# Performance work log

Hardware: AMD Instinct MI355X
Metric: run time of the kernel (lower is better)

## Reference

```python
import jax, jax.numpy as jnp
import numpy as np

DIM, SEQ, HEADS, HDIM, BATCH, VOCAB, NVOCAB = 512, 1024, 8, 64, 8, 1024, 3
EPS = 1e-5


def layer_norm(x, g, b):
    mu = x.mean(-1, keepdims=True)
    var = x.var(-1, keepdims=True)
    return (x - mu) * jax.lax.rsqrt(var + EPS) * g + b


def multiscale_retention(x, Wq, Wk, Wv, Wg, Wo):
    B, S, D = x.shape
    def split(h):  # [B,S,D] -> [B,H,S,hd]
        return h.reshape(B, S, HEADS, HDIM).transpose(0, 2, 1, 3)
    q, k, v = split(x @ Wq), split(x @ Wk), split(x @ Wv)
    # RetNet per-head decays and causal decay matrix D[h,n,m] = gamma_h^(n-m), n>=m
    gammas = 1.0 - 2.0 ** (-5.0 - jnp.arange(HEADS, dtype=jnp.float32))
    n = jnp.arange(S)
    diff = n[:, None] - n[None, :]
    decay = jnp.where(diff >= 0, gammas[:, None, None] ** jnp.maximum(diff, 0).astype(jnp.float32), 0.0)
    scores = jnp.einsum('bhsd,bhtd->bhst', q, k) * (1.0 / np.sqrt(HDIM))
    y = jnp.einsum('bhst,bhtd->bhsd', scores * decay, v)
    # group norm per head (no affine)
    mu = y.mean(-1, keepdims=True)
    var = y.var(-1, keepdims=True)
    y = (y - mu) * jax.lax.rsqrt(var + EPS)
    y = y.transpose(0, 2, 1, 3).reshape(B, S, D)
    gate = jax.nn.swish(x @ Wg)
    return (gate * y) @ Wo


def feed_forward(x, W1, b1, W2, b2):
    return jax.nn.relu(x @ W1 + b1) @ W2 + b2


def setup_inputs() -> dict:
    key = jax.random.key(0)
    ks = jax.random.split(key, 12)
    s = 0.02
    return {
        'ids': jax.random.randint(ks[0], (NVOCAB, BATCH, SEQ), 0, VOCAB),
        'emb_tables': jax.random.normal(ks[1], (NVOCAB, VOCAB, DIM), jnp.float32) * s,
        'pos_emb': jax.random.normal(ks[2], (NVOCAB, SEQ, DIM), jnp.float32) * s,
        'ln_gamma': jnp.ones((DIM,), jnp.float32),
        'ln_beta': jnp.zeros((DIM,), jnp.float32),
        'Wq': jax.random.normal(ks[3], (DIM, DIM), jnp.float32) * s,
        'Wk': jax.random.normal(ks[4], (DIM, DIM), jnp.float32) * s,
        'Wv': jax.random.normal(ks[5], (DIM, DIM), jnp.float32) * s,
        'Wg': jax.random.normal(ks[6], (DIM, DIM), jnp.float32) * s,
        'Wo': jax.random.normal(ks[7], (DIM, DIM), jnp.float32) * s,
        'W1': jax.random.normal(ks[8], (DIM, DIM), jnp.float32) * s,
        'b1': jnp.zeros((DIM,), jnp.float32),
        'W2': jax.random.normal(ks[9], (DIM, DIM), jnp.float32) * s,
        'b2': jnp.zeros((DIM,), jnp.float32),
        'fc_W': jax.random.normal(ks[10], (SEQ * DIM, 1), jnp.float32) * s,
        'fc_b': jnp.zeros((1,), jnp.float32),
    }


def reference(ids, emb_tables, pos_emb, ln_gamma, ln_beta, Wq, Wk, Wv, Wg, Wo,
              W1, b1, W2, b2, fc_W, fc_b):
    x = None
    for i in range(NVOCAB):  # loop over vocab embeddings, x overwritten each pass (as in source)
        emb = emb_tables[i][ids[i]] + pos_emb[i][None, :, :]  # [B,S,D]
        x = layer_norm(emb, ln_gamma, ln_beta)
        x = multiscale_retention(x, Wq, Wk, Wv, Wg, Wo) + x
        x = feed_forward(layer_norm(x, ln_gamma, ln_beta), W1, b1, W2, b2) + x
        x = layer_norm(x, ln_gamma, ln_beta)
    flat = x.reshape(x.shape[0], -1)  # Flatten
    return jax.nn.sigmoid(flat @ fc_W + fc_b)  # dropout inactive at inference
```

## Files before the change

### kernel.cpp

```cpp
#include <hip/hip_runtime.h>
#include <math.h>

typedef unsigned short u16;
typedef __attribute__((ext_vector_type(8))) _Float16 half8;
typedef __attribute__((ext_vector_type(4))) float f32x4;
typedef __attribute__((ext_vector_type(4))) unsigned short us4;


static __device__ __forceinline__ u16 f2h(float f) {
    _Float16 h = (_Float16)f;
    return __builtin_bit_cast(u16, h);
}
static __device__ __forceinline__ float h2f(u16 u) {
    return (float)__builtin_bit_cast(_Float16, u);
}
static __device__ __forceinline__ void gl_lds16(const void* g, void* l) {
    __builtin_amdgcn_global_load_lds(
        (const __attribute__((address_space(1))) void*)g,
        (__attribute__((address_space(3))) void*)l, 16, 0, 0);
}

__global__ __launch_bounds__(256) void prep_kernel(
    const float* __restrict__ Wq, const float* __restrict__ Wk, const float* __restrict__ Wv,
    const float* __restrict__ Wg, const float* __restrict__ Wo, const float* __restrict__ W1,
    const float* __restrict__ W2, u16* __restrict__ WT,
    const int* __restrict__ ids, const float* __restrict__ emb, const float* __restrict__ pos,
    const float* __restrict__ gam, const float* __restrict__ bet, u16* __restrict__ x0h)
{
    __shared__ float tile[64][65];
    int bx = blockIdx.x, t = threadIdx.x;
    if (bx < 448) {
        const float* Ws[7] = {Wq, Wk, Wv, Wg, Wo, W1, W2};
        int w = bx >> 6, rem = bx & 63;
        int k0 = (rem >> 3) * 64, n0 = (rem & 7) * 64;
        const float* W = Ws[w];
        for (int c = t; c < 4096; c += 256) {
            int row = c >> 6, col = c & 63;
            tile[row][col] = W[(size_t)(k0 + row) * 512 + n0 + col];
        }
        __syncthreads();
        for (int c = t; c < 4096; c += 256) {
            int row = c >> 6, col = c & 63;
            WT[(size_t)w * 262144 + (size_t)(n0 + row) * 512 + k0 + col] = f2h(tile[col][row]);
        }
    } else {
        int wid = t >> 6, lane = t & 63;
        int rbase = (bx - 448) * 8 + wid * 2;
        int col = lane * 8;
        int id0 = ids[2 * 8192 + rbase];
        int id1 = ids[2 * 8192 + rbase + 1];
        const float* pp0 = pos + (size_t)(2 * 1024 + (rbase & 1023)) * 512 + col;
        const float* pp1 = pos + (size_t)(2 * 1024 + ((rbase + 1) & 1023)) * 512 + col;
        float4 pa0 = *(const float4*)pp0, pa1 = *(const float4*)(pp0 + 4);
        float4 pb0 = *(const float4*)pp1, pb1 = *(const float4*)(pp1 + 4);
        float4 g0 = *(const float4*)&gam[col], g1 = *(const float4*)&gam[col + 4];
        float4 c0 = *(const float4*)&bet[col], c1 = *(const float4*)&bet[col + 4];
        const float* ep0 = emb + (size_t)(2 * 1024 + id0) * 512 + col;
        const float* ep1 = emb + (size_t)(2 * 1024 + id1) * 512 + col;
        float4 ea0 = *(const float4*)ep0, ea1 = *(const float4*)(ep0 + 4);
        float4 eb0 = *(const float4*)ep1, eb1 = *(const float4*)(ep1 + 4);

        float va[8] = {ea0.x + pa0.x, ea0.y + pa0.y, ea0.z + pa0.z, ea0.w + pa0.w,
                       ea1.x + pa1.x, ea1.y + pa1.y, ea1.z + pa1.z, ea1.w + pa1.w};
        float vb[8] = {eb0.x + pb0.x, eb0.y + pb0.y, eb0.z + pb0.z, eb0.w + pb0.w,
                       eb1.x + pb1.x, eb1.y + pb1.y, eb1.z + pb1.z, eb1.w + pb1.w};
        float s1a = 0.f, s2a = 0.f, s1b = 0.f, s2b = 0.f;
#pragma unroll
        for (int j = 0; j < 8; ++j) {
            s1a += va[j]; s2a += va[j] * va[j];
            s1b += vb[j]; s2b += vb[j] * vb[j];
        }
#pragma unroll
        for (int o = 32; o >= 1; o >>= 1) {
            s1a += __shfl_xor(s1a, o, 64);
            s2a += __shfl_xor(s2a, o, 64);
            s1b += __shfl_xor(s1b, o, 64);
            s2b += __shfl_xor(s2b, o, 64);
        }
        float mua = s1a * (1.f / 512.f);
        float vara = fmaxf(s2a * (1.f / 512.f) - mua * mua, 0.f);
        float rsa = 1.f / sqrtf(vara + 1e-5f);
        float mub = s1b * (1.f / 512.f);
        float varb = fmaxf(s2b * (1.f / 512.f) - mub * mub, 0.f);
        float rsb = 1.f / sqrtf(varb + 1e-5f);
        float gv[8] = {g0.x, g0.y, g0.z, g0.w, g1.x, g1.y, g1.z, g1.w};
        float bv[8] = {c0.x, c0.y, c0.z, c0.w, c1.x, c1.y, c1.z, c1.w};
        half8 ha, hb;
#pragma unroll
        for (int j = 0; j < 8; ++j) {
            ha[j] = (_Float16)((va[j] - mua) * rsa * gv[j] + bv[j]);
            hb[j] = (_Float16)((vb[j] - mub) * rsb * gv[j] + bv[j]);
        }
        *(half8*)&x0h[(size_t)rbase * 512 + col] = ha;
        *(half8*)&x0h[(size_t)(rbase + 1) * 512 + col] = hb;
    }
}

__global__ __launch_bounds__(256) void ln_kernel(
    const u16* __restrict__ xin,
    const float* __restrict__ gam, const float* __restrict__ bet,
    u16* __restrict__ outh,
    const float* __restrict__ fcW, float* __restrict__ fcpart)
{
    int wid = threadIdx.x >> 6, lane = threadIdx.x & 63;
    int row = blockIdx.x * 4 + wid;
    int col = lane * 8;
    float v[8];
    half8 x = *(const half8*)&xin[(size_t)row * 512 + col];
#pragma unroll
    for (int j = 0; j < 8; ++j) v[j] = (float)x[j];
    float s1 = 0.f, s2 = 0.f;
#pragma unroll
    for (int j = 0; j < 8; ++j) { s1 += v[j]; s2 += v[j] * v[j]; }
#pragma unroll
    for (int o = 32; o >= 1; o >>= 1) {
        s1 += __shfl_xor(s1, o, 64);
        s2 += __shfl_xor(s2, o, 64);
    }
    float mu = s1 * (1.f / 512.f);
    float var = fmaxf(s2 * (1.f / 512.f) - mu * mu, 0.f);
    float rs = 1.f / sqrtf(var + 1e-5f);
    float4 g0 = *(const float4*)&gam[col], g1 = *(const float4*)&gam[col + 4];
    float4 b0 = *(const float4*)&bet[col], b1 = *(const float4*)&bet[col + 4];
    float gv[8] = {g0.x, g0.y, g0.z, g0.w, g1.x, g1.y, g1.z, g1.w};
    float bv[8] = {b0.x, b0.y, b0.z, b0.w, b1.x, b1.y, b1.z, b1.w};
    float y[8];
#pragma unroll
    for (int j = 0; j < 8; ++j) y[j] = (v[j] - mu) * rs * gv[j] + bv[j];
    if (outh) {
        half8 hv;
#pragma unroll
        for (int j = 0; j < 8; ++j) hv[j] = (_Float16)y[j];
        *(half8*)&outh[(size_t)row * 512 + col] = hv;
    }
    if (fcW) {
        int srow = row & 1023;
        const float* wp = &fcW[(size_t)srow * 512 + col];
        float4 w0 = *(const float4*)wp, w1 = *(const float4*)(wp + 4);
        float d = y[0] * w0.x + y[1] * w0.y + y[2] * w0.z + y[3] * w0.w +
                  y[4] * w1.x + y[5] * w1.y + y[6] * w1.z + y[7] * w1.w;
#pragma unroll
        for (int o = 32; o >= 1; o >>= 1) d += __shfl_xor(d, o, 64);
        if (lane == 0) fcpart[row] = d;
    }
}

static __device__ __forceinline__ void stage_tile(
    const u16* pa0, const u16* pa1, const u16* pb0, const u16* pb1,
    u16* ldsw, int slot, int kt)
{
    int off = kt * 32;
    u16* d = ldsw + slot * 16384;
    gl_lds16(pa0 + off, d);
    gl_lds16(pa1 + off, d + 4096);
    gl_lds16(pb0 + off, d + 8192);
    gl_lds16(pb1 + off, d + 12288);
}

static __device__ __forceinline__ void compute_tile(
    const u16* lds, int slot, int wm, int wn, int quad, int l15, f32x4 (&acc)[8][4])
{
    const u16* A = lds + slot * 16384;
    const u16* B = A + 8192;
    __builtin_amdgcn_s_setprio(1);
#pragma unroll
    for (int mq = 0; mq < 2; ++mq)
#pragma unroll
        for (int nq = 0; nq < 2; ++nq) {
            half8 a[4], b[2];
#pragma unroll
            for (int i = 0; i < 4; ++i)
                a[i] = *(const half8*)&A[(wm * 128 + mq * 64 + i * 16 + l15) * 32 + quad * 8];
#pragma unroll
            for (int j = 0; j < 2; ++j)
                b[j] = *(const half8*)&B[(wn * 64 + nq * 32 + j * 16 + l15) * 32 + quad * 8];
#pragma unroll
            for (int i = 0; i < 4; ++i)
#pragma unroll
                for (int j = 0; j < 2; ++j)
                    acc[mq * 4 + i][nq * 2 + j] = __builtin_amdgcn_mfma_f32_16x16x32_f16(
                        a[i], b[j], acc[mq * 4 + i][nq * 2 + j], 0, 0, 0);
        }
    __builtin_amdgcn_s_setprio(0);
}

#define QITER(KT, VM)                                                              \
    do {                                                                           \
        if ((KT) + 3 < 16) stage_tile(pa0, pa1, pb0, pb1, ldsw, ((KT) + 3) & 3, (KT) + 3); \
        asm volatile("s_waitcnt vmcnt(" #VM ")" ::: "memory");                     \
        __builtin_amdgcn_s_barrier();                                              \
        asm volatile("" ::: "memory");                                             \
        compute_tile(lds, (KT) & 3, wm, wn, quad, l15, acc);                       \
        asm volatile("" ::: "memory");                                             \
        __builtin_amdgcn_s_barrier();                                              \
    } while (0)

__global__ __launch_bounds__(512, 2) void gemm_f16(
    const u16* __restrict__ A2, const u16* __restrict__ Bg,
    u16* __restrict__ outh, int ostride)
{
    __shared__ u16 lds[65536];
    int t = threadIdx.x;
    int wid = t >> 6, lane = t & 63, quad = lane >> 4, l15 = lane & 15;
    int wm = wid >> 2, wn = wid & 3;
    int orig = blockIdx.x;
    int wgid = (orig & 7) * 32 + (orig >> 3);
    int m0 = (wgid >> 3) * 256, n0 = (wgid & 7) * 256;

    int srow = t >> 2, sc = (t & 3) * 8;
    const u16* pa0 = A2 + (size_t)(m0 + srow) * 512 + sc;
    const u16* pa1 = pa0 + (size_t)128 * 512;
    const u16* pb0 = Bg + (size_t)(n0 + srow) * 512 + sc;
    const u16* pb1 = pb0 + (size_t)128 * 512;
    u16* ldsw = lds + wid * 512;

    f32x4 acc[8][4];
#pragma unroll
    for (int i = 0; i < 8; ++i)
#pragma unroll
        for (int j = 0; j < 4; ++j) acc[i][j] = (f32x4){0.f, 0.f, 0.f, 0.f};

    stage_tile(pa0, pa1, pb0, pb1, ldsw, 0, 0);
    stage_tile(pa0, pa1, pb0, pb1, ldsw, 1, 1);
    stage_tile(pa0, pa1, pb0, pb1, ldsw, 2, 2);

    QITER(0, 12);  QITER(1, 12);  QITER(2, 12);  QITER(3, 12);
    QITER(4, 12);  QITER(5, 12);  QITER(6, 12);  QITER(7, 12);
    QITER(8, 12);  QITER(9, 12);  QITER(10, 12); QITER(11, 12);
    QITER(12, 12);
    QITER(13, 8);  QITER(14, 4);  QITER(15, 0);

    u16* C = lds;
#pragma unroll
    for (int i = 0; i < 8; ++i)
#pragma unroll
        for (int j = 0; j < 4; ++j)
#pragma unroll
            for (int r = 0; r < 4; ++r)
                C[(wm * 128 + i * 16 + quad * 4 + r) * 256 + wn * 64 + j * 16 + l15] =
                    f2h(acc[i][j][r]);
    __builtin_amdgcn_s_barrier();
    asm volatile("" ::: "memory");
#pragma unroll
    for (int it = 0; it < 16; ++it) {
        int idx = it * 512 + t;
        int row = idx >> 5, ch = idx & 31;
        *(half8*)&outh[(size_t)(m0 + row) * ostride + n0 + ch * 8] =
            *(const half8*)&C[row * 256 + ch * 8];
    }
}

static __device__ __forceinline__ void stage_n64(
    const u16* pa, const u16* pb, u16* ldsw, int slot, int kt)
{
    int off = kt * 32;
    u16* d = ldsw + slot * 8192;
    gl_lds16(pa + off, d);
    gl_lds16(pb + off, d + 4096);
}

static __device__ __forceinline__ void compute_n64(
    const u16* lds, int slot, int wm, int wn, int quad, int l15, f32x4 (&acc)[4][2])
{
    const u16* A = lds + slot * 8192;
    const u16* B = A + 4096;
    __builtin_amdgcn_s_setprio(1);
    half8 a[4], b[2];
#pragma unroll
    for (int i = 0; i < 4; ++i)
        a[i] = *(const half8*)&A[(wm * 64 + i * 16 + l15) * 32 + quad * 8];
#pragma unroll
    for (int j = 0; j < 2; ++j)
        b[j] = *(const half8*)&B[(wn * 32 + j * 16 + l15) * 32 + quad * 8];
#pragma unroll
    for (int i = 0; i < 4; ++i)
#pragma unroll
        for (int j = 0; j < 2; ++j)
            acc[i][j] = __builtin_amdgcn_mfma_f32_16x16x32_f16(a[i], b[j], acc[i][j], 0, 0, 0);
    __builtin_amdgcn_s_setprio(0);
}

#define NITER(KT, VM)                                                          \
    do {                                                                       \
        if ((KT) + 3 < 16) stage_n64(pa, pb, ldsw, ((KT) + 3) & 3, (KT) + 3);  \
        asm volatile("s_waitcnt vmcnt(" #VM ")" ::: "memory");                 \
        __builtin_amdgcn_s_barrier();                                          \
        asm volatile("" ::: "memory");                                         \
        compute_n64(lds, (KT) & 3, wm, wn, quad, l15, acc);                    \
        asm volatile("" ::: "memory");                                         \
        __builtin_amdgcn_s_barrier();                                          \
    } while (0)

__global__ __launch_bounds__(512, 2) void gemm_f16_n64(
    const u16* __restrict__ A2, const u16* __restrict__ Bg,
    u16* __restrict__ outh,
    const u16* __restrict__ res, const float* __restrict__ bias, int mode)
{
    __shared__ u16 lds[32768];
    int t = threadIdx.x;
    int wid = t >> 6, lane = t & 63, quad = lane >> 4, l15 = lane & 15;
    int wm = wid >> 2, wn = wid & 3;
    int orig = blockIdx.x;
    int wgid = (orig & 7) * 32 + (orig >> 3);
    int m0 = (wgid >> 2) * 128, n0 = (wgid & 3) * 128;

    int srow = t >> 2, sc = (t & 3) * 8;
    const u16* pa = A2 + (size_t)(m0 + srow) * 512 + sc;
    const u16* pb = Bg + (size_t)(n0 + srow) * 512 + sc;
    u16* ldsw = lds + wid * 512;

    f32x4 acc[4][2];
#pragma unroll
    for (int i = 0; i < 4; ++i)
#pragma unroll
        for (int j = 0; j < 2; ++j) acc[i][j] = (f32x4){0.f, 0.f, 0.f, 0.f};

    stage_n64(pa, pb, ldsw, 0, 0);
    stage_n64(pa, pb, ldsw, 1, 1);
    stage_n64(pa, pb, ldsw, 2, 2);

    NITER(0, 6);  NITER(1, 6);  NITER(2, 6);  NITER(3, 6);
    NITER(4, 6);  NITER(5, 6);  NITER(6, 6);  NITER(7, 6);
    NITER(8, 6);  NITER(9, 6);  NITER(10, 6); NITER(11, 6);
    NITER(12, 6);
    NITER(13, 4); NITER(14, 2); NITER(15, 0);

#pragma unroll
    for (int i = 0; i < 4; ++i)
#pragma unroll
        for (int j = 0; j < 2; ++j) {
            int nl = wn * 32 + j * 16 + l15;
            int n = n0 + nl;
#pragma unroll
            for (int r = 0; r < 4; ++r) {
                int rl = wm * 64 + i * 16 + quad * 4 + r;
                int m = m0 + rl;
                float v = acc[i][j][r];
                if (mode == 1) v += h2f(res[(size_t)m * 512 + n]);
                else if (mode == 2) v = fmaxf(v + bias[n], 0.f);
                else if (mode == 3) v += bias[n] + h2f(res[(size_t)m * 512 + n]);
                lds[rl * 128 + nl] = f2h(v);
            }
        }
    __builtin_amdgcn_s_barrier();
    asm volatile("" ::: "memory");
#pragma unroll
    for (int it = 0; it < 4; ++it) {
        int idx = it * 512 + t;
        int row = idx >> 4, ch = idx & 15;
        *(half8*)&outh[(size_t)(m0 + row) * 512 + n0 + ch * 8] =
            *(const half8*)&lds[row * 128 + ch * 8];
    }
}

__global__ __launch_bounds__(256) void chunk_t(
    const u16* __restrict__ QKVGh, u16* __restrict__ Tst)
{
    __shared__ u16 kth[64 * 144];
    __shared__ u16 vth[64 * 144];
    int t = threadIdx.x;
    int wid = t >> 6, lane = t & 63, quad = lane >> 4, l15 = lane & 15;
    int bh = blockIdx.x >> 3, c = blockIdx.x & 7;
    int b = bh >> 3, h = bh & 7;
    float gamma = 1.f - exp2f(-(float)(5 + h));
    float l2g = log2f(gamma);

    for (int cc = t; cc < 2048; cc += 256) {
        int d = cc & 63, mseg = cc >> 6;
        size_t gbase = (size_t)(b * 1024 + c * 128 + mseg * 4) * 2048 + h * 64 + d;
        us4 k4, v4;
#pragma unroll
        for (int i = 0; i < 4; ++i) {
            float kv = h2f(QKVGh[gbase + 512 + (size_t)i * 2048]);
            k4[i] = f2h(kv * exp2f((float)(127 - (mseg * 4 + i)) * l2g));
            v4[i] = QKVGh[gbase + 1024 + (size_t)i * 2048];
        }
        int base = d * 144 + (((mseg >> 1) + d) & 15) * 8 + (mseg & 1) * 4;
        *(us4*)&kth[base] = k4;
        *(us4*)&vth[base] = v4;
    }
    __syncthreads();
    f32x4 T[4];
#pragma unroll
    for (int dt = 0; dt < 4; ++dt) T[dt] = (f32x4){0.f, 0.f, 0.f, 0.f};
    int ra = wid * 16 + l15;
#pragma unroll
    for (int ks = 0; ks < 4; ++ks) {
        half8 av = *(const half8*)&vth[ra * 144 + ((ks * 4 + quad + ra) & 15) * 8];
#pragma unroll
        for (int dt = 0; dt < 4; ++dt) {
            int rb = dt * 16 + l15;
            half8 bk = *(const half8*)&kth[rb * 144 + ((ks * 4 + quad + rb) & 15) * 8];
            T[dt] = __builtin_amdgcn_mfma_f32_16x16x32_f16(av, bk, T[dt], 0, 0, 0);
        }
    }
#pragma unroll
    for (int dt = 0; dt < 4; ++dt)
#pragma unroll
        for (int r = 0; r < 4; ++r) {
            int i = wid * 16 + quad * 4 + r;
            int j = dt * 16 + l15;
            Tst[(((size_t)bh * 8 + c) * 64 + i) * 64 + j] = f2h(T[dt][r]);
        }
}

__global__ __launch_bounds__(256) void retention_f16(
    const u16* __restrict__ QKVGh, const u16* __restrict__ Tst, u16* __restrict__ Zh)
{
    __shared__ u16 kh[128 * 64];
    __shared__ u16 vth[64 * 144];
    __shared__ u16 ph[4][16 * 132];

    int t = threadIdx.x;
    int wid = t >> 6, lane = t & 63, quad = lane >> 4, l15 = lane & 15;
    int bh = blockIdx.x >> 3, qt = blockIdx.x & 7;
    int b = bh >> 3, h = bh & 7;
    int n0 = qt * 128;

    float gamma = 1.f - exp2f(-(float)(5 + h));
    float l2g = log2f(gamma);

    {
        int srow = wid * 8 + (lane >> 3);
        int scol = (lane & 7) * 8;
#pragma unroll
        for (int i = 0; i < 4; ++i) {
            int r = i * 32 + srow;
            gl_lds16(&QKVGh[(size_t)(b * 1024 + n0 + r) * 2048 + 512 + h * 64 + scol],
                     &kh[(i * 32 + wid * 8) * 64]);
        }
    }
    for (int c = t; c < 2048; c += 256) {
        int d = c & 63, mseg = c >> 6;
        size_t gbase = (size_t)(b * 1024 + n0 + mseg * 4) * 2048 + 1024 + h * 64 + d;
        us4 v4 = {QKVGh[gbase], QKVGh[gbase + 2048],
                  QKVGh[gbase + 4096], QKVGh[gbase + 6144]};
        int base = d * 144 + (((mseg >> 1) + d) & 15) * 8 + (mseg & 1) * 4;
        *(us4*)&vth[base] = v4;
    }

    half8 aH[2][2], aHs[2][2];
#pragma unroll
    for (int g = 0; g < 2; ++g) {
        int rowloc = wid * 32 + g * 16 + l15;
        int qrow = b * 1024 + n0 + rowloc;
        const u16* qp = QKVGh + (size_t)qrow * 2048 + h * 64;
        float qs = exp2f((float)(rowloc + 1) * l2g - 3.f);
#pragma unroll
        for (int ks = 0; ks < 2; ++ks) {
            aH[g][ks] = *(const half8*)&qp[ks * 32 + quad * 8];
#pragma unroll
            for (int j = 0; j < 8; ++j)
                aHs[g][ks][j] = (_Float16)((float)aH[g][ks][j] * qs);
        }
    }

    half8 sf[2][4];
    if (qt > 0) {
        float sa[2][4][8];
#pragma unroll
        for (int ks = 0; ks < 2; ++ks)
#pragma unroll
            for (int dt = 0; dt < 4; ++dt)
#pragma unroll
                for (int j = 0; j < 8; ++j) sa[ks][dt][j] = 0.f;
        for (int c = 0; c < qt; ++c) {
            float sc = exp2f((float)(128 * (qt - 1 - c)) * l2g);
            const u16* tp = &Tst[((size_t)bh * 8 + c) * 4096];
#pragma unroll
            for (int ks = 0; ks < 2; ++ks)
#pragma unroll
                for (int dt = 0; dt < 4; ++dt) {
                    half8 tv = *(const half8*)&tp[(dt * 16 + l15) * 64 + ks * 32 + quad * 8];
#pragma unroll
                    for (int j = 0; j < 8; ++j) sa[ks][dt][j] += sc * (float)tv[j];
                }
        }
#pragma unroll
        for (int ks = 0; ks < 2; ++ks)
#pragma unroll
            for (int dt = 0; dt < 4; ++dt)
#pragma unroll
                for (int j = 0; j < 8; ++j) sf[ks][dt][j] = (_Float16)sa[ks][dt][j];
    }
    __syncthreads();

    f32x4 yacc[2][4];
#pragma unroll
    for (int g = 0; g < 2; ++g)
#pragma unroll
        for (int dt = 0; dt < 4; ++dt) yacc[g][dt] = (f32x4){0.f, 0.f, 0.f, 0.f};

    if (qt > 0) {
#pragma unroll
        for (int ks = 0; ks < 2; ++ks)
#pragma unroll
            for (int g = 0; g < 2; ++g)
#pragma unroll
                for (int dt = 0; dt < 4; ++dt)
                    yacc[g][dt] = __builtin_amdgcn_mfma_f32_16x16x32_f16(aHs[g][ks], sf[ks][dt], yacc[g][dt], 0, 0, 0);
    }

#pragma unroll
    for (int g = 0; g < 2; ++g) {
        f32x4 sacc[8];
#pragma unroll
        for (int tn = 0; tn < 8; ++tn) sacc[tn] = (f32x4){0.f, 0.f, 0.f, 0.f};
#pragma unroll
        for (int tn = 0; tn < 8; ++tn)
#pragma unroll
            for (int ks = 0; ks < 2; ++ks) {
                half8 bH = *(const half8*)&kh[(tn * 16 + l15) * 64 + ks * 32 + quad * 8];
                sacc[tn] = __builtin_amdgcn_mfma_f32_16x16x32_f16(aH[g][ks], bH, sacc[tn], 0, 0, 0);
            }
#pragma unroll
        for (int tn = 0; tn < 8; ++tn) {
            int mloc = tn * 16 + l15;
#pragma unroll
            for (int r = 0; r < 4; ++r) {
                int nloc = wid * 32 + g * 16 + quad * 4 + r;
                int diff = nloc - mloc;
                float p = (diff >= 0) ? sacc[tn][r] * exp2f((float)diff * l2g - 3.0f) : 0.f;
                ph[wid][(quad * 4 + r) * 132 + tn * 16 + l15] = f2h(p);
            }
        }
        half8 pH[4];
#pragma unroll
        for (int ks = 0; ks < 4; ++ks)
            pH[ks] = *(const half8*)&ph[wid][l15 * 132 + ks * 32 + quad * 8];
#pragma unroll
        for (int dt = 0; dt < 4; ++dt) {
            int d = dt * 16 + l15;
#pragma unroll
            for (int ks = 0; ks < 4; ++ks) {
                half8 vv = *(const half8*)&vth[d * 144 + ((ks * 4 + quad + d) & 15) * 8];
                yacc[g][dt] = __builtin_amdgcn_mfma_f32_16x16x32_f16(pH[ks], vv, yacc[g][dt], 0, 0, 0);
            }
        }
    }

#pragma unroll
    for (int g = 0; g < 2; ++g) {
#pragma unroll
        for (int r = 0; r < 4; ++r) {
            float s1 = yacc[g][0][r] + yacc[g][1][r] + yacc[g][2][r] + yacc[g][3][r];
            float s2 = yacc[g][0][r] * yacc[g][0][r] + yacc[g][1][r] * yacc[g][1][r] +
                       yacc[g][2][r] * yacc[g][2][r] + yacc[g][3][r] * yacc[g][3][r];
#pragma unroll
            for (int o = 1; o <= 8; o <<= 1) {
                s1 += __shfl_xor(s1, o, 64);
                s2 += __shfl_xor(s2, o, 64);
            }
            float mu = s1 * (1.f / 64.f);
            float var = fmaxf(s2 * (1.f / 64.f) - mu * mu, 0.f);
            float rs = 1.f / sqrtf(var + 1e-5f);
            int nglob = n0 + wid * 32 + g * 16 + quad * 4 + r;
            size_t grow = (size_t)(b * 1024 + nglob);
#pragma unroll
            for (int dt = 0; dt < 4; ++dt) {
                int d = dt * 16 + l15;
                float yv = (yacc[g][dt][r] - mu) * rs;
                float gt = h2f(QKVGh[grow * 2048 + 1536 + h * 64 + d]);
                float sw = gt / (1.f + expf(-gt));
                Zh[grow * 512 + h * 64 + d] = f2h(yv * sw);
            }
        }
    }
}

__global__ __launch_bounds__(256) void fc_final(const float* __restrict__ fcpart,
                                                const float* __restrict__ fcb,
                                                float* __restrict__ out)
{
    __shared__ float red[4];
    int b = blockIdx.x, t = threadIdx.x;
    float4 v = *(const float4*)&fcpart[(size_t)b * 1024 + t * 4];
    float s = v.x + v.y + v.z + v.w;
    int wid = t >> 6, lane = t & 63;
#pragma unroll
    for (int o = 32; o >= 1; o >>= 1) s += __shfl_xor(s, o, 64);
    if (lane == 0) red[wid] = s;
    __syncthreads();
    if (t == 0) {
        float l = red[0] + red[1] + red[2] + red[3] + fcb[0];
        out[b] = 1.f / (1.f + expf(-l));
    }
}

extern "C" void kernel_launch(void* const* d_in, const int* in_sizes, int n_in,
                              void* d_out, int out_size, void* d_ws, size_t ws_size,
                              hipStream_t stream)
{
    const int* ids = (const int*)d_in[0];
    const float* emb = (const float*)d_in[1];
    const float* pos = (const float*)d_in[2];
    const float* ln_g = (const float*)d_in[3];
    const float* ln_b = (const float*)d_in[4];
    const float* Wq = (const float*)d_in[5];
    const float* Wk = (const float*)d_in[6];
    const float* Wv = (const float*)d_in[7];
    const float* Wg = (const float*)d_in[8];
    const float* Wo = (const float*)d_in[9];
    const float* W1 = (const float*)d_in[10];
    const float* b1 = (const float*)d_in[11];
    const float* W2 = (const float*)d_in[12];
    const float* b2 = (const float*)d_in[13];
    const float* fcW = (const float*)d_in[14];
    const float* fcb = (const float*)d_in[15];
    float* out = (float*)d_out;

    char* ws = (char*)d_ws;
    u16* WT     = (u16*)(ws);
    u16* x0h    = (u16*)(ws + 3670016);
    u16* Zh     = (u16*)(ws + 12058624);
    u16* QKVGh  = (u16*)(ws + 20447232);
    float* fcpart = (float*)(ws + 54001664);
    u16* Tst    = (u16*)(ws + 54034432);
    u16* X1h = QKVGh;
    u16* Th  = (u16*)((char*)QKVGh + 8388608);
    u16* Hh  = (u16*)((char*)QKVGh + 16777216);
    u16* X2h = Zh;

    prep_kernel<<<1472, 256, 0, stream>>>(Wq, Wk, Wv, Wg, Wo, W1, W2, WT,
                                          ids, emb, pos, ln_g, ln_b, x0h);
    gemm_f16<<<256, 512, 0, stream>>>(x0h, WT, QKVGh, 2048);
    chunk_t<<<512, 256, 0, stream>>>(QKVGh, Tst);
    retention_f16<<<512, 256, 0, stream>>>(QKVGh, Tst, Zh);
    gemm_f16_n64<<<256, 512, 0, stream>>>(Zh, WT + 4 * 262144, X1h, x0h, nullptr, 1);
    ln_kernel<<<2048, 256, 0, stream>>>(X1h, ln_g, ln_b, Th, nullptr, nullptr);
    gemm_f16_n64<<<256, 512, 0, stream>>>(Th, WT + 5 * 262144, Hh, nullptr, b1, 2);
    gemm_f16_n64<<<256, 512, 0, stream>>>(Hh, WT + 6 * 262144, X2h, X1h, b2, 3);
    ln_kernel<<<2048, 256, 0, stream>>>(X2h, ln_g, ln_b, nullptr, fcW, fcpart);
    fc_final<<<8, 256, 0, stream>>>(fcpart, fcb, out);
}
```

Measured before the change: 208.8 us.

## Fuse post-retention GEMMs, layernorms and FC into one cooperative persistent kernel

```diff
diff --git a/kernel.cpp b/kernel.cpp
--- a/kernel.cpp
+++ b/kernel.cpp
@@ -1,5 +1,8 @@
 #include <hip/hip_runtime.h>
+#include <hip/hip_cooperative_groups.h>
 #include <math.h>
+
+namespace cg = cooperative_groups;
 
 typedef unsigned short u16;
 typedef __attribute__((ext_vector_type(8))) _Float16 half8;
@@ -96,55 +99,6 @@
     }
 }
 
-__global__ __launch_bounds__(256) void ln_kernel(
-    const u16* __restrict__ xin,
-    const float* __restrict__ gam, const float* __restrict__ bet,
-    u16* __restrict__ outh,
-    const float* __restrict__ fcW, float* __restrict__ fcpart)
-{
-    int wid = threadIdx.x >> 6, lane = threadIdx.x & 63;
-    int row = blockIdx.x * 4 + wid;
-    int col = lane * 8;
-    float v[8];
-    half8 x = *(const half8*)&xin[(size_t)row * 512 + col];
-#pragma unroll
-    for (int j = 0; j < 8; ++j) v[j] = (float)x[j];
-    float s1 = 0.f, s2 = 0.f;
-#pragma unroll
-    for (int j = 0; j < 8; ++j) { s1 += v[j]; s2 += v[j] * v[j]; }
-#pragma unroll
-    for (int o = 32; o >= 1; o >>= 1) {
-        s1 += __shfl_xor(s1, o, 64);
-        s2 += __shfl_xor(s2, o, 64);
-    }
-    float mu = s1 * (1.f / 512.f);
-    float var = fmaxf(s2 * (1.f / 512.f) - mu * mu, 0.f);
-    float rs = 1.f / sqrtf(var + 1e-5f);
-    float4 g0 = *(const float4*)&gam[col], g1 = *(const float4*)&gam[col + 4];
-    float4 b0 = *(const float4*)&bet[col], b1 = *(const float4*)&bet[col + 4];
-    float gv[8] = {g0.x, g0.y, g0.z, g0.w, g1.x, g1.y, g1.z, g1.w};
-    float bv[8] = {b0.x, b0.y, b0.z, b0.w, b1.x, b1.y, b1.z, b1.w};
-    float y[8];
-#pragma unroll
-    for (int j = 0; j < 8; ++j) y[j] = (v[j] - mu) * rs * gv[j] + bv[j];
-    if (outh) {
-        half8 hv;
-#pragma unroll
-        for (int j = 0; j < 8; ++j) hv[j] = (_Float16)y[j];
-        *(half8*)&outh[(size_t)row * 512 + col] = hv;
-    }
-    if (fcW) {
-        int srow = row & 1023;
-        const float* wp = &fcW[(size_t)srow * 512 + col];
-        float4 w0 = *(const float4*)wp, w1 = *(const float4*)(wp + 4);
-        float d = y[0] * w0.x + y[1] * w0.y + y[2] * w0.z + y[3] * w0.w +
-                  y[4] * w1.x + y[5] * w1.y + y[6] * w1.z + y[7] * w1.w;
-#pragma unroll
-        for (int o = 32; o >= 1; o >>= 1) d += __shfl_xor(d, o, 64);
-        if (lane == 0) fcpart[row] = d;
-    }
-}
-
 static __device__ __forceinline__ void stage_tile(
     const u16* pa0, const u16* pa1, const u16* pb0, const u16* pb1,
     u16* ldsw, int slot, int kt)
@@ -291,12 +245,12 @@
         __builtin_amdgcn_s_barrier();                                          \
     } while (0)
 
-__global__ __launch_bounds__(512, 2) void gemm_f16_n64(
+template <int MODE>
+static __device__ __forceinline__ void gemm_stage(
     const u16* __restrict__ A2, const u16* __restrict__ Bg,
-    u16* __restrict__ outh,
-    const u16* __restrict__ res, const float* __restrict__ bias, int mode)
-{
-    __shared__ u16 lds[32768];
+    u16* __restrict__ outh, const u16* __restrict__ res,
+    const float* __restrict__ bias, u16* lds)
+{
     int t = threadIdx.x;
     int wid = t >> 6, lane = t & 63, quad = lane >> 4, l15 = lane & 15;
     int wm = wid >> 2, wn = wid & 3;
@@ -336,9 +290,9 @@
                 int rl = wm * 64 + i * 16 + quad * 4 + r;
                 int m = m0 + rl;
                 float v = acc[i][j][r];
-                if (mode == 1) v += h2f(res[(size_t)m * 512 + n]);
-                else if (mode == 2) v = fmaxf(v + bias[n], 0.f);
-                else if (mode == 3) v += bias[n] + h2f(res[(size_t)m * 512 + n]);
+                if (MODE == 1) v += h2f(res[(size_t)m * 512 + n]);
+                else if (MODE == 2) v = fmaxf(v + bias[n], 0.f);
+                else if (MODE == 3) v += bias[n] + h2f(res[(size_t)m * 512 + n]);
                 lds[rl * 128 + nl] = f2h(v);
             }
         }
@@ -350,6 +304,97 @@
         int row = idx >> 4, ch = idx & 15;
         *(half8*)&outh[(size_t)(m0 + row) * 512 + n0 + ch * 8] =
             *(const half8*)&lds[row * 128 + ch * 8];
+    }
+}
+
+static __device__ __forceinline__ void ln_stage(
+    const u16* __restrict__ xin, const float* __restrict__ gam,
+    const float* __restrict__ bet, u16* __restrict__ outh,
+    const float* __restrict__ fcW, float* __restrict__ fcpart)
+{
+    int wid = threadIdx.x >> 6, lane = threadIdx.x & 63;
+    int col = lane * 8;
+    float4 g0 = *(const float4*)&gam[col], g1 = *(const float4*)&gam[col + 4];
+    float4 c0 = *(const float4*)&bet[col], c1 = *(const float4*)&bet[col + 4];
+    float gv[8] = {g0.x, g0.y, g0.z, g0.w, g1.x, g1.y, g1.z, g1.w};
+    float bv[8] = {c0.x, c0.y, c0.z, c0.w, c1.x, c1.y, c1.z, c1.w};
+#pragma unroll
+    for (int rr = 0; rr < 4; ++rr) {
+        int row = blockIdx.x * 32 + wid * 4 + rr;
+        float v[8];
+        half8 x = *(const half8*)&xin[(size_t)row * 512 + col];
+#pragma unroll
+        for (int j = 0; j < 8; ++j) v[j] = (float)x[j];
+        float s1 = 0.f, s2 = 0.f;
+#pragma unroll
+        for (int j = 0; j < 8; ++j) { s1 += v[j]; s2 += v[j] * v[j]; }
+#pragma unroll
+        for (int o = 32; o >= 1; o >>= 1) {
+            s1 += __shfl_xor(s1, o, 64);
+            s2 += __shfl_xor(s2, o, 64);
+        }
+        float mu = s1 * (1.f / 512.f);
+        float var = fmaxf(s2 * (1.f / 512.f) - mu * mu, 0.f);
+        float rs = 1.f / sqrtf(var + 1e-5f);
+        float y[8];
+#pragma unroll
+        for (int j = 0; j < 8; ++j) y[j] = (v[j] - mu) * rs * gv[j] + bv[j];
+        if (outh) {
+            half8 hv;
+#pragma unroll
+            for (int j = 0; j < 8; ++j) hv[j] = (_Float16)y[j];
+            *(half8*)&outh[(size_t)row * 512 + col] = hv;
+        }
+        if (fcW) {
+            int srow = row & 1023;
+            const float* wp = &fcW[(size_t)srow * 512 + col];
+            float4 w0 = *(const float4*)wp, w1 = *(const float4*)(wp + 4);
+            float d = y[0] * w0.x + y[1] * w0.y + y[2] * w0.z + y[3] * w0.w +
+                      y[4] * w1.x + y[5] * w1.y + y[6] * w1.z + y[7] * w1.w;
+#pragma unroll
+            for (int o = 32; o >= 1; o >>= 1) d += __shfl_xor(d, o, 64);
+            if (lane == 0) fcpart[row] = d;
+        }
+    }
+}
+
+__global__ __launch_bounds__(512, 2) void tail_fused(
+    const u16* __restrict__ Zh, const u16* __restrict__ WT,
+    const u16* __restrict__ x0h, u16* __restrict__ X1h,
+    u16* __restrict__ Th, u16* __restrict__ Hh, u16* __restrict__ X2h,
+    const float* __restrict__ b1v, const float* __restrict__ b2v,
+    const float* __restrict__ gam, const float* __restrict__ bet,
+    const float* __restrict__ fcW, float* __restrict__ fcpart,
+    const float* __restrict__ fcb, float* __restrict__ out)
+{
+    cg::grid_group grid = cg::this_grid();
+    __shared__ u16 lds[32768];
+
+    gemm_stage<1>(Zh, WT + 4 * 262144, X1h, x0h, nullptr, lds);
+    grid.sync();
+    ln_stage(X1h, gam, bet, Th, nullptr, nullptr);
+    grid.sync();
+    gemm_stage<2>(Th, WT + 5 * 262144, Hh, nullptr, b1v, lds);
+    grid.sync();
+    gemm_stage<3>(Hh, WT + 6 * 262144, X2h, X1h, b2v, lds);
+    grid.sync();
+    ln_stage(X2h, gam, bet, nullptr, fcW, fcpart);
+    grid.sync();
+    if (blockIdx.x < 8) {
+        int b = blockIdx.x, t = threadIdx.x;
+        float* red = (float*)lds;
+        float2 v = *(const float2*)&fcpart[(size_t)b * 1024 + t * 2];
+        float s = v.x + v.y;
+        int wid = t >> 6, lane = t & 63;
+#pragma unroll
+        for (int o = 32; o >= 1; o >>= 1) s += __shfl_xor(s, o, 64);
+        if (lane == 0) red[wid] = s;
+        __syncthreads();
+        if (t == 0) {
+            float l = red[0] + red[1] + red[2] + red[3] +
+                      red[4] + red[5] + red[6] + red[7] + fcb[0];
+            out[b] = 1.f / (1.f + expf(-l));
+        }
     }
 }
 
@@ -565,25 +610,6 @@
                 Zh[grow * 512 + h * 64 + d] = f2h(yv * sw);
             }
         }
-    }
-}
-
-__global__ __launch_bounds__(256) void fc_final(const float* __restrict__ fcpart,
-                                                const float* __restrict__ fcb,
-                                                float* __restrict__ out)
-{
-    __shared__ float red[4];
-    int b = blockIdx.x, t = threadIdx.x;
-    float4 v = *(const float4*)&fcpart[(size_t)b * 1024 + t * 4];
-    float s = v.x + v.y + v.z + v.w;
-    int wid = t >> 6, lane = t & 63;
-#pragma unroll
-    for (int o = 32; o >= 1; o >>= 1) s += __shfl_xor(s, o, 64);
-    if (lane == 0) red[wid] = s;
-    __syncthreads();
-    if (t == 0) {
-        float l = red[0] + red[1] + red[2] + red[3] + fcb[0];
-        out[b] = 1.f / (1.f + expf(-l));
     }
 }
 
@@ -626,10 +652,15 @@
     gemm_f16<<<256, 512, 0, stream>>>(x0h, WT, QKVGh, 2048);
     chunk_t<<<512, 256, 0, stream>>>(QKVGh, Tst);
     retention_f16<<<512, 256, 0, stream>>>(QKVGh, Tst, Zh);
-    gemm_f16_n64<<<256, 512, 0, stream>>>(Zh, WT + 4 * 262144, X1h, x0h, nullptr, 1);
-    ln_kernel<<<2048, 256, 0, stream>>>(X1h, ln_g, ln_b, Th, nullptr, nullptr);
-    gemm_f16_n64<<<256, 512, 0, stream>>>(Th, WT + 5 * 262144, Hh, nullptr, b1, 2);
-    gemm_f16_n64<<<256, 512, 0, stream>>>(Hh, WT + 6 * 262144, X2h, X1h, b2, 3);
-    ln_kernel<<<2048, 256, 0, stream>>>(X2h, ln_g, ln_b, nullptr, fcW, fcpart);
-    fc_final<<<8, 256, 0, stream>>>(fcpart, fcb, out);
-}
+
+    const u16* Zh_c = Zh;
+    const u16* WT_c = WT;
+    const u16* x0h_c = x0h;
+    void* args[] = {
+        (void*)&Zh_c, (void*)&WT_c, (void*)&x0h_c,
+        (void*)&X1h, (void*)&Th, (void*)&Hh, (void*)&X2h,
+        (void*)&b1, (void*)&b2, (void*)&ln_g, (void*)&ln_b,
+        (void*)&fcW, (void*)&fcpart, (void*)&fcb, (void*)&out};
+    hipLaunchCooperativeKernel((const void*)tail_fused, dim3(256), dim3(512),
+                               args, 0, stream);
+}
```

Measured after the change: 378.5 us. 1.81x slower.

## Precompute chunk state prefix scan in separate kernel for retention

Applied to the files above, without the earlier changes.

```diff
diff --git a/kernel.cpp b/kernel.cpp
--- a/kernel.cpp
+++ b/kernel.cpp
@@ -404,8 +404,28 @@
         }
 }
 
+__global__ __launch_bounds__(256) void tscan(
+    const u16* __restrict__ Tst, u16* __restrict__ Sst)
+{
+    int bh = blockIdx.x >> 3, p = blockIdx.x & 7;
+    int h = bh & 7;
+    float gamma = 1.f - exp2f(-(float)(5 + h));
+    float g128 = exp2f(128.f * log2f(gamma));
+    int e = p * 512 + threadIdx.x * 2;
+    const u16* tp = Tst + (size_t)bh * 32768 + e;
+    u16* sp = Sst + (size_t)bh * 32768 + e;
+    float s0 = 0.f, s1 = 0.f;
+#pragma unroll
+    for (int c = 0; c < 8; ++c) {
+        sp[c * 4096] = f2h(s0);
+        sp[c * 4096 + 1] = f2h(s1);
+        s0 = g128 * s0 + h2f(tp[c * 4096]);
+        s1 = g128 * s1 + h2f(tp[c * 4096 + 1]);
+    }
+}
+
 __global__ __launch_bounds__(256) void retention_f16(
-    const u16* __restrict__ QKVGh, const u16* __restrict__ Tst, u16* __restrict__ Zh)
+    const u16* __restrict__ QKVGh, const u16* __restrict__ Sst, u16* __restrict__ Zh)
 {
     __shared__ u16 kh[128 * 64];
     __shared__ u16 vth[64 * 144];
@@ -456,50 +476,29 @@
     }
 
     half8 sf[2][4];
-    if (qt > 0) {
-        float sa[2][4][8];
+    {
+        const u16* sp = &Sst[((size_t)bh * 8 + qt) * 4096];
 #pragma unroll
         for (int ks = 0; ks < 2; ++ks)
 #pragma unroll
             for (int dt = 0; dt < 4; ++dt)
-#pragma unroll
-                for (int j = 0; j < 8; ++j) sa[ks][dt][j] = 0.f;
-        for (int c = 0; c < qt; ++c) {
-            float sc = exp2f((float)(128 * (qt - 1 - c)) * l2g);
-            const u16* tp = &Tst[((size_t)bh * 8 + c) * 4096];
-#pragma unroll
-            for (int ks = 0; ks < 2; ++ks)
-#pragma unroll
-                for (int dt = 0; dt < 4; ++dt) {
-                    half8 tv = *(const half8*)&tp[(dt * 16 + l15) * 64 + ks * 32 + quad * 8];
-#pragma unroll
-                    for (int j = 0; j < 8; ++j) sa[ks][dt][j] += sc * (float)tv[j];
-                }
-        }
-#pragma unroll
-        for (int ks = 0; ks < 2; ++ks)
+                sf[ks][dt] = *(const half8*)&sp[(dt * 16 + l15) * 64 + ks * 32 + quad * 8];
+    }
+    __syncthreads();
+
+    f32x4 yacc[2][4];
+#pragma unroll
+    for (int g = 0; g < 2; ++g)
+#pragma unroll
+        for (int dt = 0; dt < 4; ++dt) yacc[g][dt] = (f32x4){0.f, 0.f, 0.f, 0.f};
+
+#pragma unroll
+    for (int ks = 0; ks < 2; ++ks)
+#pragma unroll
+        for (int g = 0; g < 2; ++g)
 #pragma unroll
             for (int dt = 0; dt < 4; ++dt)
-#pragma unroll
-                for (int j = 0; j < 8; ++j) sf[ks][dt][j] = (_Float16)sa[ks][dt][j];
-    }
-    __syncthreads();
-
-    f32x4 yacc[2][4];
-#pragma unroll
-    for (int g = 0; g < 2; ++g)
-#pragma unroll
-        for (int dt = 0; dt < 4; ++dt) yacc[g][dt] = (f32x4){0.f, 0.f, 0.f, 0.f};
-
-    if (qt > 0) {
-#pragma unroll
-        for (int ks = 0; ks < 2; ++ks)
-#pragma unroll
-            for (int g = 0; g < 2; ++g)
-#pragma unroll
-                for (int dt = 0; dt < 4; ++dt)
-                    yacc[g][dt] = __builtin_amdgcn_mfma_f32_16x16x32_f16(aHs[g][ks], sf[ks][dt], yacc[g][dt], 0, 0, 0);
-    }
+                yacc[g][dt] = __builtin_amdgcn_mfma_f32_16x16x32_f16(aHs[g][ks], sf[ks][dt], yacc[g][dt], 0, 0, 0);
 
 #pragma unroll
     for (int g = 0; g < 2; ++g) {
@@ -616,6 +615,7 @@
     u16* QKVGh  = (u16*)(ws + 20447232);
     float* fcpart = (float*)(ws + 54001664);
     u16* Tst    = (u16*)(ws + 54034432);
+    u16* Sst    = (u16*)(ws + 58228736);
     u16* X1h = QKVGh;
     u16* Th  = (u16*)((char*)QKVGh + 8388608);
     u16* Hh  = (u16*)((char*)QKVGh + 16777216);
@@ -625,7 +625,8 @@
                                           ids, emb, pos, ln_g, ln_b, x0h);
     gemm_f16<<<256, 512, 0, stream>>>(x0h, WT, QKVGh, 2048);
     chunk_t<<<512, 256, 0, stream>>>(QKVGh, Tst);
-    retention_f16<<<512, 256, 0, stream>>>(QKVGh, Tst, Zh);
+    tscan<<<512, 256, 0, stream>>>(Tst, Sst);
+    retention_f16<<<512, 256, 0, stream>>>(QKVGh, Sst, Zh);
     gemm_f16_n64<<<256, 512, 0, stream>>>(Zh, WT + 4 * 262144, X1h, x0h, nullptr, 1);
     ln_kernel<<<2048, 256, 0, stream>>>(X1h, ln_g, ln_b, Th, nullptr, nullptr);
     gemm_f16_n64<<<256, 512, 0, stream>>>(Th, WT + 5 * 262144, Hh, nullptr, b1, 2);
```

Measured after the change: 204.4 us. -2.1%, faster.
